# Optimization experiments

Measured on AMD Instinct MI355X. Metric: run time of the kernel, lower is better.

Reference implementation:

```python
import jax, jax.numpy as jnp
import numpy as np


def setup_inputs() -> dict:
    key = jax.random.key(0)
    kq, kk, kv, kl = jax.random.split(key, 4)
    B, Nq, Nk, D, Dv = 16, 2048, 2048, 128, 128
    queries = jax.random.normal(kq, (B, Nq, D), dtype=jnp.float32)
    keys = jax.random.normal(kk, (B, Nk, D), dtype=jnp.float32)
    values = jax.random.normal(kv, (B, Nk, Dv), dtype=jnp.float32)
    valid_lens = jax.random.randint(kl, (B,), 0, 2048, dtype=jnp.int64)
    return {"queries": queries, "keys": keys, "values": values, "valid_lens": valid_lens}


def reference(queries, keys, values, valid_lens):
    # queries: (B, Nq, d), keys: (B, Nk, d), values: (B, Nk, dv), valid_lens: (B,)
    d = queries.shape[-1]
    scores = jnp.einsum('bqd,bkd->bqk', queries, keys) / jnp.sqrt(jnp.asarray(d, queries.dtype))
    # masked_softmax: original sets masked score positions to 1e-8 (NOT -inf) before softmax
    nk = scores.shape[-1]
    mask = jnp.arange(nk)[None, :] < valid_lens[:, None]  # (B, Nk)
    scores = jnp.where(mask[:, None, :], scores, jnp.asarray(1e-8, scores.dtype))
    attn = jax.nn.softmax(scores, axis=-1)
    # dropout rate 0.0 -> identity (eval semantics)
    return jnp.einsum('bqk,bkv->bqv', attn, values)
```

## Files before the change

kernel.cpp:

```cpp
#include <hip/hip_runtime.h>
#include <stdint.h>

#define BATCH 16
#define NQ    2048
#define NK    2048
#define DD    128
#define DVV   128

typedef __bf16 bf16_t;
typedef __bf16 bf16x2 __attribute__((ext_vector_type(2)));
typedef __bf16 bf16x4 __attribute__((ext_vector_type(4)));
typedef __bf16 bf16x8 __attribute__((ext_vector_type(8)));
typedef float  f32x4  __attribute__((ext_vector_type(4)));

#define KB_OFF   ((size_t)0)
#define VT_OFF   ((size_t)8 * 1024 * 1024)
#define SUF_OFF  ((size_t)16 * 1024 * 1024)
#define SCH_OFF  (SUF_OFF + 65536)
#define WS_NEED  (SCH_OFF + 4096)

__device__ __forceinline__ int load_valid_len(const int* VL, int b) {
  bool looks64 = true;
#pragma unroll
  for (int i = 0; i < 16; ++i) {
    int hi = VL[2 * i + 1];
    unsigned lo = (unsigned)VL[2 * i];
    looks64 = looks64 && (hi == 0) && (lo <= 2048u);
  }
  int L = looks64 ? VL[2 * b] : VL[b];
  return min(max(L, 0), NK);
}

__device__ __forceinline__ void gld16(const void* g, void* l) {
  __builtin_amdgcn_global_load_lds(
      (const __attribute__((address_space(1))) unsigned int*)g,
      (__attribute__((address_space(3))) unsigned int*)l, 16, 0, 0);
}

__device__ __forceinline__ f32x4 mfma16(bf16x8 a, bf16x8 b, f32x4 c) {
  return __builtin_amdgcn_mfma_f32_16x16x32_bf16(a, b, c, 0, 0, 0);
}

__global__ void prep_kernel(const float* __restrict__ K, const float* __restrict__ V,
                            const int* __restrict__ VL,
                            bf16_t* __restrict__ Kb, bf16_t* __restrict__ Vt,
                            float* __restrict__ sufV, int* __restrict__ sched) {
  __shared__ bf16_t tile[128 * 72];
  __shared__ int bs[16];
  const int bid = blockIdx.x;
  const int t = threadIdx.x;
  if (bid < 512) {
#pragma unroll
    for (int i = 0; i < 4; ++i) {
      size_t f4 = (size_t)bid * 2048 + (size_t)i * 512 + 2 * t;
      float4 a = ((const float4*)K)[f4];
      float4 c = ((const float4*)K)[f4 + 1];
      bf16x8 o;
      o[0] = (bf16_t)a.x; o[1] = (bf16_t)a.y; o[2] = (bf16_t)a.z; o[3] = (bf16_t)a.w;
      o[4] = (bf16_t)c.x; o[5] = (bf16_t)c.y; o[6] = (bf16_t)c.z; o[7] = (bf16_t)c.w;
      ((bf16x8*)Kb)[f4 >> 1] = o;
    }
    return;
  }
  if (bid < 1024) {
    int v = bid - 512;
    int b = v & 15, kt = v >> 4;
    int L = load_valid_len(VL, b);
    int m = t & 31;
    int g = t >> 5;
    int r2 = m * 2;
    int k0g = kt * 64 + r2;
    const float* src = V + ((size_t)b * NK + k0g) * DVV;
    float sacc[4][4];
#pragma unroll
    for (int i = 0; i < 4; ++i)
#pragma unroll
      for (int j = 0; j < 4; ++j) sacc[i][j] = 0.f;
    bool a0 = (k0g >= L), a1 = (k0g + 1 >= L);
#pragma unroll
    for (int i = 0; i < 4; ++i) {
      int d4 = g * 4 + i * 32;
      float4 u0 = *(const float4*)(src + d4);
      float4 u1 = *(const float4*)(src + DVV + d4);
      *(bf16x2*)&tile[(d4 + 0) * 72 + r2] = (bf16x2){(bf16_t)u0.x, (bf16_t)u1.x};
      *(bf16x2*)&tile[(d4 + 1) * 72 + r2] = (bf16x2){(bf16_t)u0.y, (bf16_t)u1.y};
      *(bf16x2*)&tile[(d4 + 2) * 72 + r2] = (bf16x2){(bf16_t)u0.z, (bf16_t)u1.z};
      *(bf16x2*)&tile[(d4 + 3) * 72 + r2] = (bf16x2){(bf16_t)u0.w, (bf16_t)u1.w};
      if (a0) { sacc[i][0] += u0.x; sacc[i][1] += u0.y; sacc[i][2] += u0.z; sacc[i][3] += u0.w; }
      if (a1) { sacc[i][0] += u1.x; sacc[i][1] += u1.y; sacc[i][2] += u1.z; sacc[i][3] += u1.w; }
    }
    __syncthreads();
#pragma unroll
    for (int off = 1; off < 32; off <<= 1)
#pragma unroll
      for (int i = 0; i < 4; ++i)
#pragma unroll
        for (int j = 0; j < 4; ++j) sacc[i][j] += __shfl_xor(sacc[i][j], off, 64);
    if (m == 0) {
#pragma unroll
      for (int i = 0; i < 4; ++i)
#pragma unroll
        for (int j = 0; j < 4; ++j)
          atomicAdd(&sufV[b * 128 + g * 4 + i * 32 + j], sacc[i][j]);
    }
    int dv = t >> 1, half = t & 1;
    bf16_t* dst = Vt + (size_t)b * DVV * NK + (size_t)dv * NK + kt * 64 + half * 32;
    const bf16_t* srow = &tile[dv * 72 + half * 32];
#pragma unroll
    for (int j = 0; j < 4; ++j)
      *(bf16x8*)(dst + j * 8) = *(const bf16x8*)(srow + j * 8);
    return;
  }
  if (t == 0) {
    int Ls[16], idx[16];
#pragma unroll
    for (int i = 0; i < 16; ++i) { Ls[i] = load_valid_len(VL, i); idx[i] = i; }
    for (int i = 1; i < 16; ++i) {
      int lv = Ls[i], iv = idx[i], j = i - 1;
      while (j >= 0 && Ls[j] < lv) { Ls[j + 1] = Ls[j]; idx[j + 1] = idx[j]; --j; }
      Ls[j + 1] = lv; idx[j + 1] = iv;
    }
#pragma unroll
    for (int i = 0; i < 16; ++i) bs[i] = idx[i];
  }
  __syncthreads();
  for (int j = t; j < 512; j += 256) {
    int r = (j < 256) ? j : (767 - j);
    sched[j] = (bs[r >> 5] << 5) | (r & 31);
  }
}

__launch_bounds__(256, 2)
__global__ void attn_kernel(const float* __restrict__ Q, const bf16_t* __restrict__ Kb,
                            const bf16_t* __restrict__ Vt, const int* __restrict__ VL,
                            const float* __restrict__ sufV, const int* __restrict__ sched,
                            float* __restrict__ Out) {
  __shared__ __align__(16) char smem[73728];
  bf16_t* sK = (bf16_t*)smem;
  bf16_t* sV = (bf16_t*)(smem + 32768);

  const int unit = sched[blockIdx.x];
  const int b  = (unit >> 5) & 15;
  const int qt = unit & 31;
  const int L  = load_valid_len(VL, b);
  const int ktiles = (L + 63) >> 6;

  const int tid = threadIdx.x;
  const int wave = tid >> 6;
  const int lane = tid & 63;
  const int col = lane & 15;
  const int quad = lane >> 4;
  const int wr = wave >> 1;
  const int wc = wave & 1;

  bf16_t* pw = (bf16_t*)(smem + 65536 + wave * 2048);

  bf16x8 qf[2][4];
  {
    const float scq = 0.1275174307f;
#pragma unroll
    for (int m = 0; m < 2; ++m) {
      const float* qrow = Q + ((size_t)b * NQ + qt * 64 + wr * 32 + m * 16 + col) * DD + quad * 8;
#pragma unroll
      for (int ks = 0; ks < 4; ++ks) {
        float4 u0 = *(const float4*)(qrow + ks * 32);
        float4 u1 = *(const float4*)(qrow + ks * 32 + 4);
        bf16x8 f;
        f[0] = (bf16_t)(u0.x * scq); f[1] = (bf16_t)(u0.y * scq);
        f[2] = (bf16_t)(u0.z * scq); f[3] = (bf16_t)(u0.w * scq);
        f[4] = (bf16_t)(u1.x * scq); f[5] = (bf16_t)(u1.y * scq);
        f[6] = (bf16_t)(u1.z * scq); f[7] = (bf16_t)(u1.w * scq);
        qf[m][ks] = f;
      }
    }
  }

  const char* Kbyte = (const char*)Kb + (size_t)b * NK * DD * 2;
  const char* Vbyte = (const char*)Vt + (size_t)b * DVV * NK * 2;
  int koff[4], voff[4];
#pragma unroll
  for (int i = 0; i < 4; ++i) {
    int krow = wave * 16 + i * 4 + (lane >> 4);
    koff[i] = krow * 256 + (((lane & 15) ^ (krow & 15)) * 16);
    int vrow = wave * 32 + i * 8 + (lane >> 3);
    voff[i] = vrow * (NK * 2) + (((lane & 7) ^ ((lane >> 3) & 7)) * 16);
  }

  f32x4 Oacc[2][8];
#pragma unroll
  for (int m = 0; m < 2; ++m)
#pragma unroll
    for (int o = 0; o < 8; ++o) Oacc[m][o] = (f32x4){0.f, 0.f, 0.f, 0.f};
  float lsum[2][4];
#pragma unroll
  for (int m = 0; m < 2; ++m)
#pragma unroll
    for (int r = 0; r < 4; ++r) lsum[m][r] = 0.f;

  auto issueTile = [&](int kt, int bufi) {
    const char* kb = Kbyte + (size_t)kt * 16384;
    const char* vb = Vbyte + (size_t)kt * 128;
    bf16_t* kl = sK + bufi * 8192 + wave * 2048;
    bf16_t* vl = sV + bufi * 8192 + wave * 2048;
#pragma unroll
    for (int i = 0; i < 4; ++i) {
      gld16(kb + koff[i], kl + i * 512);
      gld16(vb + voff[i], vl + i * 512);
    }
  };

  if (ktiles > 0) issueTile(0, 0);
  int bufi = 0;
  for (int kt = 0; kt < ktiles; ++kt) {
    if (kt + 1 < ktiles) {
      issueTile(kt + 1, bufi ^ 1);
      asm volatile("s_waitcnt vmcnt(8)\n\ts_barrier" ::: "memory");
    } else {
      asm volatile("s_waitcnt vmcnt(0)\n\ts_barrier" ::: "memory");
    }

    const bf16_t* kb_ = sK + bufi * 8192;
    const bf16_t* vb_ = sV + bufi * 8192;

    f32x4 sc[2][2];
#pragma unroll
    for (int m = 0; m < 2; ++m)
#pragma unroll
      for (int nt = 0; nt < 2; ++nt) sc[m][nt] = (f32x4){0.f, 0.f, 0.f, 0.f};
#pragma unroll
    for (int ks = 0; ks < 4; ++ks) {
#pragma unroll
      for (int nt = 0; nt < 2; ++nt) {
        bf16x8 bb = *(const bf16x8*)&kb_[(wc * 32 + nt * 16 + col) * 128 + (((ks * 4 + quad) ^ col) * 8)];
        sc[0][nt] = mfma16(qf[0][ks], bb, sc[0][nt]);
        sc[1][nt] = mfma16(qf[1][ks], bb, sc[1][nt]);
      }
    }

    const int key0 = kt * 64 + wc * 32;
#pragma unroll
    for (int nt = 0; nt < 2; ++nt) {
      bool valid = (key0 + nt * 16 + col) < L;
#pragma unroll
      for (int m = 0; m < 2; ++m)
#pragma unroll
        for (int r = 0; r < 4; ++r) {
          float p = __builtin_amdgcn_exp2f(sc[m][nt][r]);
          p = valid ? p : 0.f;
          lsum[m][r] += p;
          int prow = quad * 4 + r;
          int cidx = m * 4 + nt * 2 + (col >> 3);
          int phys = cidx ^ (prow & 7);
          pw[prow * 64 + phys * 8 + (col & 7)] = (bf16_t)p;
        }
    }

    bf16x8 pa[2];
#pragma unroll
    for (int m = 0; m < 2; ++m)
      pa[m] = *(const bf16x8*)&pw[col * 64 + (((m * 4 + quad) ^ (col & 7)) * 8)];
#pragma unroll
    for (int o = 0; o < 8; ++o) {
      bf16x8 bb = *(const bf16x8*)&vb_[(o * 16 + col) * 64 + (((wc * 4 + quad) ^ (col & 7)) * 8)];
      Oacc[0][o] = mfma16(pa[0], bb, Oacc[0][o]);
      Oacc[1][o] = mfma16(pa[1], bb, Oacc[1][o]);
    }
    asm volatile("s_barrier" ::: "memory");
    bufi ^= 1;
  }

#pragma unroll
  for (int off = 1; off < 16; off <<= 1)
#pragma unroll
    for (int m = 0; m < 2; ++m)
#pragma unroll
      for (int r = 0; r < 4; ++r) lsum[m][r] += __shfl_xor(lsum[m][r], off, 64);

  float* scrO = (float*)(smem + wr * 18432);
  float* scrL = (float*)(smem + 65536) + wr * 32;

  if (wc == 1) {
#pragma unroll
    for (int m = 0; m < 2; ++m)
#pragma unroll
      for (int o = 0; o < 8; ++o)
        *(f32x4*)&scrO[(o * 16 + col) * 36 + m * 16 + quad * 4] = Oacc[m][o];
    if (col == 0) {
#pragma unroll
      for (int m = 0; m < 2; ++m)
#pragma unroll
        for (int r = 0; r < 4; ++r) scrL[m * 16 + quad * 4 + r] = lsum[m][r];
    }
  }
  __syncthreads();
  if (wc == 0) {
    const float wmask = (float)(NK - L);
    float invl[2][4];
#pragma unroll
    for (int m = 0; m < 2; ++m)
#pragma unroll
      for (int r = 0; r < 4; ++r)
        invl[m][r] = 1.0f / (lsum[m][r] + scrL[m * 16 + quad * 4 + r] + wmask);
    const float* sfv = sufV + b * DVV;
    float* Ob = Out + ((size_t)b * NQ + qt * 64 + wr * 32) * DVV;
#pragma unroll
    for (int m = 0; m < 2; ++m)
#pragma unroll
      for (int o = 0; o < 8; ++o) {
        f32x4 part = *(const f32x4*)&scrO[(o * 16 + col) * 36 + m * 16 + quad * 4];
        float svv = sfv[o * 16 + col];
#pragma unroll
        for (int r = 0; r < 4; ++r)
          Ob[(size_t)(m * 16 + quad * 4 + r) * DVV + o * 16 + col] =
              (Oacc[m][o][r] + part[r] + svv) * invl[m][r];
      }
  }
}

#define KSTR 152
#define VSTR 88
#define PSTR 72

__global__ void suffix_fb(const float* __restrict__ V, const int* __restrict__ VL,
                          float* __restrict__ ws) {
  int b = blockIdx.x;
  int kc = blockIdx.y;
  int L = load_valid_len(VL, b);
  int k0 = kc * 128, k1 = k0 + 128;
  int lo = max(L, k0);
  int t = threadIdx.x;
  int dv = t & 127;
  int h = t >> 7;
  float s = 0.f;
  for (int k = lo + h; k < k1; k += 2)
    s += V[((size_t)b * NK + k) * DVV + dv];
  __shared__ float part[128];
  if (h == 0) part[dv] = s;
  __syncthreads();
  if (h == 1) atomicAdd(&ws[b * DVV + dv], part[dv] + s);
}

__launch_bounds__(256, 2)
__global__ void attn_fb(const float* __restrict__ Q, const float* __restrict__ K,
                        const float* __restrict__ V, const int* __restrict__ VL,
                        const float* __restrict__ sufV, float* __restrict__ Out) {
  const int flat = blockIdx.x;
  const int b  = flat & 15;
  const int qt = flat >> 4;
  const int L  = load_valid_len(VL, b);

  __shared__ bf16_t sK2[64 * KSTR];
  __shared__ bf16_t sVT2[128 * VSTR];
  __shared__ bf16_t sP2[4 * 16 * PSTR];

  const int tid  = threadIdx.x;
  const int wave = tid >> 6;
  const int lane = tid & 63;
  const int col  = lane & 15;
  const int quad = lane >> 4;

  const float* Qb = Q + ((size_t)b * NQ + qt * 64 + wave * 16) * DD;
  const float* Kb = K + (size_t)b * NK * DD;
  const float* Vb = V + (size_t)b * NK * DVV;

  bf16x8 qf[4];
  {
    const float scq = 0.08838834764831845f;
    const float* qrow = Qb + (size_t)col * DD + quad * 8;
#pragma unroll
    for (int ks = 0; ks < 4; ++ks) {
      float4 u0 = *(const float4*)(qrow + ks * 32);
      float4 u1 = *(const float4*)(qrow + ks * 32 + 4);
      bf16x8 f;
      f[0] = (bf16_t)(u0.x * scq); f[1] = (bf16_t)(u0.y * scq);
      f[2] = (bf16_t)(u0.z * scq); f[3] = (bf16_t)(u0.w * scq);
      f[4] = (bf16_t)(u1.x * scq); f[5] = (bf16_t)(u1.y * scq);
      f[6] = (bf16_t)(u1.z * scq); f[7] = (bf16_t)(u1.w * scq);
      qf[ks] = f;
    }
  }

  f32x4 Oacc[8];
#pragma unroll
  for (int o = 0; o < 8; ++o) Oacc[o] = (f32x4){0.f, 0.f, 0.f, 0.f};
  float m_i[4], l_i[4];
#pragma unroll
  for (int r = 0; r < 4; ++r) { m_i[r] = -1e30f; l_i[r] = 0.f; }

  const int ktiles = (L + 63) >> 6;
  for (int kt = 0; kt < ktiles; ++kt) {
    {
      int r0 = tid >> 5;
      int d4 = (tid & 31) * 4;
      const float* src = Kb + ((size_t)(kt * 64) + r0) * DD + d4;
#pragma unroll
      for (int i = 0; i < 8; ++i) {
        float4 u = *(const float4*)(src + (size_t)i * 8 * DD);
        bf16x4 w4 = {(bf16_t)u.x, (bf16_t)u.y, (bf16_t)u.z, (bf16_t)u.w};
        *(bf16x4*)&sK2[(r0 + i * 8) * KSTR + d4] = w4;
      }
    }
    {
      int r2 = (tid & 31) * 2;
      int dbase = (tid >> 5) * 4;
#pragma unroll
      for (int i = 0; i < 4; ++i) {
        int d4 = dbase + i * 32;
        const float* s0 = Vb + ((size_t)(kt * 64) + r2) * DVV + d4;
        float4 u0 = *(const float4*)s0;
        float4 u1 = *(const float4*)(s0 + DVV);
        *(bf16x2*)&sVT2[(d4 + 0) * VSTR + r2] = (bf16x2){(bf16_t)u0.x, (bf16_t)u1.x};
        *(bf16x2*)&sVT2[(d4 + 1) * VSTR + r2] = (bf16x2){(bf16_t)u0.y, (bf16_t)u1.y};
        *(bf16x2*)&sVT2[(d4 + 2) * VSTR + r2] = (bf16x2){(bf16_t)u0.z, (bf16_t)u1.z};
        *(bf16x2*)&sVT2[(d4 + 3) * VSTR + r2] = (bf16x2){(bf16_t)u0.w, (bf16_t)u1.w};
      }
    }
    __syncthreads();

    f32x4 sv4[4];
#pragma unroll
    for (int nt = 0; nt < 4; ++nt) sv4[nt] = (f32x4){0.f, 0.f, 0.f, 0.f};
#pragma unroll
    for (int ks = 0; ks < 4; ++ks) {
      bf16x8 a = qf[ks];
#pragma unroll
      for (int nt = 0; nt < 4; ++nt) {
        bf16x8 bb = *(const bf16x8*)&sK2[(nt * 16 + col) * KSTR + ks * 32 + quad * 8];
        sv4[nt] = mfma16(a, bb, sv4[nt]);
      }
    }

    const int key0 = kt * 64;
    float sv[4][4];
    float mloc[4] = {-1e30f, -1e30f, -1e30f, -1e30f};
#pragma unroll
    for (int nt = 0; nt < 4; ++nt) {
      int key = key0 + nt * 16 + col;
      bool valid = key < L;
#pragma unroll
      for (int r = 0; r < 4; ++r) {
        float v = valid ? sv4[nt][r] : -1e30f;
        sv[nt][r] = v;
        mloc[r] = fmaxf(mloc[r], v);
      }
    }
#pragma unroll
    for (int off = 1; off < 16; off <<= 1)
#pragma unroll
      for (int r = 0; r < 4; ++r) mloc[r] = fmaxf(mloc[r], __shfl_xor(mloc[r], off, 64));
    float al[4];
#pragma unroll
    for (int r = 0; r < 4; ++r) {
      float mn = fmaxf(m_i[r], mloc[r]);
      al[r] = __expf(m_i[r] - mn);
      m_i[r] = mn;
    }
    float lloc[4] = {0.f, 0.f, 0.f, 0.f};
#pragma unroll
    for (int nt = 0; nt < 4; ++nt)
#pragma unroll
      for (int r = 0; r < 4; ++r) {
        float p = __expf(sv[nt][r] - m_i[r]);
        sv[nt][r] = p;
        lloc[r] += p;
      }
#pragma unroll
    for (int off = 1; off < 16; off <<= 1)
#pragma unroll
      for (int r = 0; r < 4; ++r) lloc[r] += __shfl_xor(lloc[r], off, 64);
#pragma unroll
    for (int r = 0; r < 4; ++r) l_i[r] = l_i[r] * al[r] + lloc[r];
#pragma unroll
    for (int o = 0; o < 8; ++o)
#pragma unroll
      for (int r = 0; r < 4; ++r) Oacc[o][r] *= al[r];

    bf16_t* pw = &sP2[wave * 16 * PSTR];
#pragma unroll
    for (int nt = 0; nt < 4; ++nt)
#pragma unroll
      for (int r = 0; r < 4; ++r)
        pw[(quad * 4 + r) * PSTR + nt * 16 + col] = (bf16_t)sv[nt][r];

#pragma unroll
    for (int ks2 = 0; ks2 < 2; ++ks2) {
      bf16x8 a = *(const bf16x8*)&pw[(lane & 15) * PSTR + ks2 * 32 + quad * 8];
#pragma unroll
      for (int o = 0; o < 8; ++o) {
        bf16x8 bb = *(const bf16x8*)&sVT2[(o * 16 + col) * VSTR + ks2 * 32 + quad * 8];
        Oacc[o] = mfma16(a, bb, Oacc[o]);
      }
    }
    __syncthreads();
  }

  if (L < NK) {
    const float c = 1e-8f;
    const float w = (float)(NK - L);
    float a2[4], ec[4];
#pragma unroll
    for (int r = 0; r < 4; ++r) {
      float mn = fmaxf(m_i[r], c);
      a2[r] = __expf(m_i[r] - mn);
      ec[r] = __expf(c - mn);
      l_i[r] = l_i[r] * a2[r] + w * ec[r];
    }
    const float* sfv = sufV + b * DVV;
#pragma unroll
    for (int o = 0; o < 8; ++o) {
      float svv = sfv[o * 16 + col];
#pragma unroll
      for (int r = 0; r < 4; ++r) Oacc[o][r] = Oacc[o][r] * a2[r] + ec[r] * svv;
    }
  }

  float invl[4];
#pragma unroll
  for (int r = 0; r < 4; ++r) invl[r] = 1.0f / l_i[r];

  float* Ob = Out + ((size_t)b * NQ + qt * 64 + wave * 16) * DVV;
#pragma unroll
  for (int o = 0; o < 8; ++o)
#pragma unroll
    for (int r = 0; r < 4; ++r)
      Ob[(size_t)(quad * 4 + r) * DVV + o * 16 + col] = Oacc[o][r] * invl[r];
}

extern "C" void kernel_launch(void* const* d_in, const int* in_sizes, int n_in,
                              void* d_out, int out_size, void* d_ws, size_t ws_size,
                              hipStream_t stream) {
  const float* Q  = (const float*)d_in[0];
  const float* K  = (const float*)d_in[1];
  const float* V  = (const float*)d_in[2];
  const int*   VL = (const int*)d_in[3];
  float* out = (float*)d_out;

  if (ws_size >= WS_NEED) {
    char* ws = (char*)d_ws;
    bf16_t* Kb = (bf16_t*)(ws + KB_OFF);
    bf16_t* Vt = (bf16_t*)(ws + VT_OFF);
    float* sufV = (float*)(ws + SUF_OFF);
    int* sched = (int*)(ws + SCH_OFF);

    hipMemsetAsync(sufV, 0, BATCH * DVV * sizeof(float), stream);
    prep_kernel<<<1025, 256, 0, stream>>>(K, V, VL, Kb, Vt, sufV, sched);
    attn_kernel<<<512, 256, 0, stream>>>(Q, Kb, Vt, VL, sufV, sched, out);
  } else {
    float* ws = (float*)d_ws;
    hipMemsetAsync(ws, 0, BATCH * DVV * sizeof(float), stream);
    dim3 g1(BATCH, 16);
    suffix_fb<<<g1, 256, 0, stream>>>(V, VL, ws);
    attn_fb<<<BATCH * (NQ / 64), 256, 0, stream>>>(Q, K, V, VL, ws, out);
  }
}
```

Baseline: 139.0 us.

## Widen attention blocks to 8 waves splitting 128-key tiles four ways

```diff
diff --git a/kernel.cpp b/kernel.cpp
--- a/kernel.cpp
+++ b/kernel.cpp
@@ -124,36 +124,34 @@
     for (int i = 0; i < 16; ++i) bs[i] = idx[i];
   }
   __syncthreads();
-  for (int j = t; j < 512; j += 256) {
-    int r = (j < 256) ? j : (767 - j);
-    sched[j] = (bs[r >> 5] << 5) | (r & 31);
-  }
-}
-
-__launch_bounds__(256, 2)
+  for (int j = t; j < 512; j += 256)
+    sched[j] = (bs[j >> 5] << 5) | (j & 31);
+}
+
+__launch_bounds__(512, 1)
 __global__ void attn_kernel(const float* __restrict__ Q, const bf16_t* __restrict__ Kb,
                             const bf16_t* __restrict__ Vt, const int* __restrict__ VL,
                             const float* __restrict__ sufV, const int* __restrict__ sched,
                             float* __restrict__ Out) {
-  __shared__ __align__(16) char smem[73728];
+  __shared__ __align__(16) char smem[147456];
   bf16_t* sK = (bf16_t*)smem;
-  bf16_t* sV = (bf16_t*)(smem + 32768);
+  bf16_t* sV = (bf16_t*)(smem + 65536);
 
   const int unit = sched[blockIdx.x];
   const int b  = (unit >> 5) & 15;
   const int qt = unit & 31;
   const int L  = load_valid_len(VL, b);
-  const int ktiles = (L + 63) >> 6;
+  const int ktiles = (L + 127) >> 7;
 
   const int tid = threadIdx.x;
   const int wave = tid >> 6;
   const int lane = tid & 63;
   const int col = lane & 15;
   const int quad = lane >> 4;
-  const int wr = wave >> 1;
-  const int wc = wave & 1;
-
-  bf16_t* pw = (bf16_t*)(smem + 65536 + wave * 2048);
+  const int wr = wave >> 2;
+  const int wc = wave & 3;
+
+  bf16_t* pw = (bf16_t*)(smem + 131072 + wave * 2048);
 
   bf16x8 qf[2][4];
   {
@@ -182,8 +180,8 @@
   for (int i = 0; i < 4; ++i) {
     int krow = wave * 16 + i * 4 + (lane >> 4);
     koff[i] = krow * 256 + (((lane & 15) ^ (krow & 15)) * 16);
-    int vrow = wave * 32 + i * 8 + (lane >> 3);
-    voff[i] = vrow * (NK * 2) + (((lane & 7) ^ ((lane >> 3) & 7)) * 16);
+    int vrow = wave * 16 + i * 4 + (lane >> 4);
+    voff[i] = vrow * (NK * 2) + (((lane & 15) ^ (vrow & 15)) * 16);
   }
 
   f32x4 Oacc[2][8];
@@ -198,10 +196,10 @@
     for (int r = 0; r < 4; ++r) lsum[m][r] = 0.f;
 
   auto issueTile = [&](int kt, int bufi) {
-    const char* kb = Kbyte + (size_t)kt * 16384;
-    const char* vb = Vbyte + (size_t)kt * 128;
-    bf16_t* kl = sK + bufi * 8192 + wave * 2048;
-    bf16_t* vl = sV + bufi * 8192 + wave * 2048;
+    const char* kb = Kbyte + (size_t)kt * 32768;
+    const char* vb = Vbyte + (size_t)kt * 256;
+    bf16_t* kl = sK + bufi * 16384 + wave * 2048;
+    bf16_t* vl = sV + bufi * 16384 + wave * 2048;
 #pragma unroll
     for (int i = 0; i < 4; ++i) {
       gld16(kb + koff[i], kl + i * 512);
@@ -219,8 +217,8 @@
       asm volatile("s_waitcnt vmcnt(0)\n\ts_barrier" ::: "memory");
     }
 
-    const bf16_t* kb_ = sK + bufi * 8192;
-    const bf16_t* vb_ = sV + bufi * 8192;
+    const bf16_t* kb_ = sK + bufi * 16384;
+    const bf16_t* vb_ = sV + bufi * 16384;
 
     f32x4 sc[2][2];
 #pragma unroll
@@ -237,7 +235,7 @@
       }
     }
 
-    const int key0 = kt * 64 + wc * 32;
+    const int key0 = kt * 128 + wc * 32;
 #pragma unroll
     for (int nt = 0; nt < 2; ++nt) {
       bool valid = (key0 + nt * 16 + col) < L;
@@ -261,7 +259,7 @@
       pa[m] = *(const bf16x8*)&pw[col * 64 + (((m * 4 + quad) ^ (col & 7)) * 8)];
 #pragma unroll
     for (int o = 0; o < 8; ++o) {
-      bf16x8 bb = *(const bf16x8*)&vb_[(o * 16 + col) * 64 + (((wc * 4 + quad) ^ (col & 7)) * 8)];
+      bf16x8 bb = *(const bf16x8*)&vb_[(o * 16 + col) * 128 + (((wc * 4 + quad) ^ col) * 8)];
       Oacc[0][o] = mfma16(pa[0], bb, Oacc[0][o]);
       Oacc[1][o] = mfma16(pa[1], bb, Oacc[1][o]);
     }
@@ -276,10 +274,9 @@
 #pragma unroll
       for (int r = 0; r < 4; ++r) lsum[m][r] += __shfl_xor(lsum[m][r], off, 64);
 
-  float* scrO = (float*)(smem + wr * 18432);
-  float* scrL = (float*)(smem + 65536) + wr * 32;
-
-  if (wc == 1) {
+  if (wc) {
+    float* scrO = (float*)smem + (size_t)(wr * 3 + (wc - 1)) * 4608;
+    float* scrL = (float*)(smem + 131072) + (wr * 3 + (wc - 1)) * 32;
 #pragma unroll
     for (int m = 0; m < 2; ++m)
 #pragma unroll
@@ -299,20 +296,29 @@
 #pragma unroll
     for (int m = 0; m < 2; ++m)
 #pragma unroll
-      for (int r = 0; r < 4; ++r)
-        invl[m][r] = 1.0f / (lsum[m][r] + scrL[m * 16 + quad * 4 + r] + wmask);
+      for (int r = 0; r < 4; ++r) {
+        float lt = lsum[m][r] + wmask;
+#pragma unroll
+        for (int s = 0; s < 3; ++s)
+          lt += ((float*)(smem + 131072))[(wr * 3 + s) * 32 + m * 16 + quad * 4 + r];
+        invl[m][r] = 1.0f / lt;
+      }
     const float* sfv = sufV + b * DVV;
     float* Ob = Out + ((size_t)b * NQ + qt * 64 + wr * 32) * DVV;
 #pragma unroll
     for (int m = 0; m < 2; ++m)
 #pragma unroll
       for (int o = 0; o < 8; ++o) {
-        f32x4 part = *(const f32x4*)&scrO[(o * 16 + col) * 36 + m * 16 + quad * 4];
+        f32x4 acc = Oacc[m][o];
+#pragma unroll
+        for (int s = 0; s < 3; ++s)
+          acc += *(const f32x4*)&((float*)smem)[(size_t)(wr * 3 + s) * 4608 +
+                                               (o * 16 + col) * 36 + m * 16 + quad * 4];
         float svv = sfv[o * 16 + col];
 #pragma unroll
         for (int r = 0; r < 4; ++r)
           Ob[(size_t)(m * 16 + quad * 4 + r) * DVV + o * 16 + col] =
-              (Oacc[m][o][r] + part[r] + svv) * invl[m][r];
+              (acc[r] + svv) * invl[m][r];
       }
   }
 }
@@ -544,7 +550,7 @@
 
     hipMemsetAsync(sufV, 0, BATCH * DVV * sizeof(float), stream);
     prep_kernel<<<1025, 256, 0, stream>>>(K, V, VL, Kb, Vt, sufV, sched);
-    attn_kernel<<<512, 256, 0, stream>>>(Q, Kb, Vt, VL, sufV, sched, out);
+    attn_kernel<<<512, 512, 0, stream>>>(Q, Kb, Vt, VL, sufV, sched, out);
   } else {
     float* ws = (float*)d_ws;
     hipMemsetAsync(ws, 0, BATCH * DVV * sizeof(float), stream);
```

Measured after the change: 146.4 us. +5.3%, slower.

## Use 8 waves per block with 16-row query groups and MFMA priority hints

Applied to the files above, without the earlier changes.

```diff
diff --git a/kernel.cpp b/kernel.cpp
--- a/kernel.cpp
+++ b/kernel.cpp
@@ -124,18 +124,16 @@
     for (int i = 0; i < 16; ++i) bs[i] = idx[i];
   }
   __syncthreads();
-  for (int j = t; j < 512; j += 256) {
-    int r = (j < 256) ? j : (767 - j);
-    sched[j] = (bs[r >> 5] << 5) | (r & 31);
-  }
-}
-
-__launch_bounds__(256, 2)
+  for (int j = t; j < 512; j += 256)
+    sched[j] = (bs[j >> 5] << 5) | (j & 31);
+}
+
+__launch_bounds__(512, 4)
 __global__ void attn_kernel(const float* __restrict__ Q, const bf16_t* __restrict__ Kb,
                             const bf16_t* __restrict__ Vt, const int* __restrict__ VL,
                             const float* __restrict__ sufV, const int* __restrict__ sched,
                             float* __restrict__ Out) {
-  __shared__ __align__(16) char smem[73728];
+  __shared__ __align__(16) char smem[81920];
   bf16_t* sK = (bf16_t*)smem;
   bf16_t* sV = (bf16_t*)(smem + 32768);
 
@@ -150,60 +148,51 @@
   const int lane = tid & 63;
   const int col = lane & 15;
   const int quad = lane >> 4;
-  const int wr = wave >> 1;
-  const int wc = wave & 1;
+  const int qg = wave >> 1;
+  const int kg = wave & 1;
 
   bf16_t* pw = (bf16_t*)(smem + 65536 + wave * 2048);
 
-  bf16x8 qf[2][4];
+  bf16x8 qf[4];
   {
     const float scq = 0.1275174307f;
-#pragma unroll
-    for (int m = 0; m < 2; ++m) {
-      const float* qrow = Q + ((size_t)b * NQ + qt * 64 + wr * 32 + m * 16 + col) * DD + quad * 8;
-#pragma unroll
-      for (int ks = 0; ks < 4; ++ks) {
-        float4 u0 = *(const float4*)(qrow + ks * 32);
-        float4 u1 = *(const float4*)(qrow + ks * 32 + 4);
-        bf16x8 f;
-        f[0] = (bf16_t)(u0.x * scq); f[1] = (bf16_t)(u0.y * scq);
-        f[2] = (bf16_t)(u0.z * scq); f[3] = (bf16_t)(u0.w * scq);
-        f[4] = (bf16_t)(u1.x * scq); f[5] = (bf16_t)(u1.y * scq);
-        f[6] = (bf16_t)(u1.z * scq); f[7] = (bf16_t)(u1.w * scq);
-        qf[m][ks] = f;
-      }
+    const float* qrow = Q + ((size_t)b * NQ + qt * 64 + qg * 16 + col) * DD + quad * 8;
+#pragma unroll
+    for (int ks = 0; ks < 4; ++ks) {
+      float4 u0 = *(const float4*)(qrow + ks * 32);
+      float4 u1 = *(const float4*)(qrow + ks * 32 + 4);
+      bf16x8 f;
+      f[0] = (bf16_t)(u0.x * scq); f[1] = (bf16_t)(u0.y * scq);
+      f[2] = (bf16_t)(u0.z * scq); f[3] = (bf16_t)(u0.w * scq);
+      f[4] = (bf16_t)(u1.x * scq); f[5] = (bf16_t)(u1.y * scq);
+      f[6] = (bf16_t)(u1.z * scq); f[7] = (bf16_t)(u1.w * scq);
+      qf[ks] = f;
     }
   }
 
   const char* Kbyte = (const char*)Kb + (size_t)b * NK * DD * 2;
   const char* Vbyte = (const char*)Vt + (size_t)b * DVV * NK * 2;
-  int koff[4], voff[4];
-#pragma unroll
-  for (int i = 0; i < 4; ++i) {
-    int krow = wave * 16 + i * 4 + (lane >> 4);
+  int koff[2], voff[2];
+#pragma unroll
+  for (int i = 0; i < 2; ++i) {
+    int krow = wave * 8 + i * 4 + quad;
     koff[i] = krow * 256 + (((lane & 15) ^ (krow & 15)) * 16);
-    int vrow = wave * 32 + i * 8 + (lane >> 3);
-    voff[i] = vrow * (NK * 2) + (((lane & 7) ^ ((lane >> 3) & 7)) * 16);
-  }
-
-  f32x4 Oacc[2][8];
-#pragma unroll
-  for (int m = 0; m < 2; ++m)
-#pragma unroll
-    for (int o = 0; o < 8; ++o) Oacc[m][o] = (f32x4){0.f, 0.f, 0.f, 0.f};
-  float lsum[2][4];
-#pragma unroll
-  for (int m = 0; m < 2; ++m)
-#pragma unroll
-    for (int r = 0; r < 4; ++r) lsum[m][r] = 0.f;
+    int vrow = wave * 16 + i * 8 + (lane >> 3);
+    voff[i] = vrow * (NK * 2) + (((lane & 7) ^ (vrow & 7)) * 16);
+  }
+
+  f32x4 Oacc[8];
+#pragma unroll
+  for (int o = 0; o < 8; ++o) Oacc[o] = (f32x4){0.f, 0.f, 0.f, 0.f};
+  float lsum[4] = {0.f, 0.f, 0.f, 0.f};
 
   auto issueTile = [&](int kt, int bufi) {
     const char* kb = Kbyte + (size_t)kt * 16384;
     const char* vb = Vbyte + (size_t)kt * 128;
-    bf16_t* kl = sK + bufi * 8192 + wave * 2048;
-    bf16_t* vl = sV + bufi * 8192 + wave * 2048;
-#pragma unroll
-    for (int i = 0; i < 4; ++i) {
+    bf16_t* kl = sK + bufi * 8192 + wave * 1024;
+    bf16_t* vl = sV + bufi * 8192 + wave * 1024;
+#pragma unroll
+    for (int i = 0; i < 2; ++i) {
       gld16(kb + koff[i], kl + i * 512);
       gld16(vb + voff[i], vl + i * 512);
     }
@@ -214,7 +203,7 @@
   for (int kt = 0; kt < ktiles; ++kt) {
     if (kt + 1 < ktiles) {
       issueTile(kt + 1, bufi ^ 1);
-      asm volatile("s_waitcnt vmcnt(8)\n\ts_barrier" ::: "memory");
+      asm volatile("s_waitcnt vmcnt(4)\n\ts_barrier" ::: "memory");
     } else {
       asm volatile("s_waitcnt vmcnt(0)\n\ts_barrier" ::: "memory");
     }
@@ -222,49 +211,44 @@
     const bf16_t* kb_ = sK + bufi * 8192;
     const bf16_t* vb_ = sV + bufi * 8192;
 
-    f32x4 sc[2][2];
-#pragma unroll
-    for (int m = 0; m < 2; ++m)
-#pragma unroll
-      for (int nt = 0; nt < 2; ++nt) sc[m][nt] = (f32x4){0.f, 0.f, 0.f, 0.f};
+    f32x4 sc[2];
+#pragma unroll
+    for (int nt = 0; nt < 2; ++nt) sc[nt] = (f32x4){0.f, 0.f, 0.f, 0.f};
+    __builtin_amdgcn_s_setprio(1);
 #pragma unroll
     for (int ks = 0; ks < 4; ++ks) {
 #pragma unroll
       for (int nt = 0; nt < 2; ++nt) {
-        bf16x8 bb = *(const bf16x8*)&kb_[(wc * 32 + nt * 16 + col) * 128 + (((ks * 4 + quad) ^ col) * 8)];
-        sc[0][nt] = mfma16(qf[0][ks], bb, sc[0][nt]);
-        sc[1][nt] = mfma16(qf[1][ks], bb, sc[1][nt]);
-      }
-    }
-
-    const int key0 = kt * 64 + wc * 32;
+        bf16x8 bb = *(const bf16x8*)&kb_[(kg * 32 + nt * 16 + col) * 128 + (((ks * 4 + quad) ^ col) * 8)];
+        sc[nt] = mfma16(qf[ks], bb, sc[nt]);
+      }
+    }
+    __builtin_amdgcn_s_setprio(0);
+
+    const int key0 = kt * 64 + kg * 32;
 #pragma unroll
     for (int nt = 0; nt < 2; ++nt) {
       bool valid = (key0 + nt * 16 + col) < L;
 #pragma unroll
-      for (int m = 0; m < 2; ++m)
-#pragma unroll
-        for (int r = 0; r < 4; ++r) {
-          float p = __builtin_amdgcn_exp2f(sc[m][nt][r]);
-          p = valid ? p : 0.f;
-          lsum[m][r] += p;
-          int prow = quad * 4 + r;
-          int cidx = m * 4 + nt * 2 + (col >> 3);
-          int phys = cidx ^ (prow & 7);
-          pw[prow * 64 + phys * 8 + (col & 7)] = (bf16_t)p;
-        }
-    }
-
-    bf16x8 pa[2];
-#pragma unroll
-    for (int m = 0; m < 2; ++m)
-      pa[m] = *(const bf16x8*)&pw[col * 64 + (((m * 4 + quad) ^ (col & 7)) * 8)];
+      for (int r = 0; r < 4; ++r) {
+        float p = __builtin_amdgcn_exp2f(sc[nt][r]);
+        p = valid ? p : 0.f;
+        lsum[r] += p;
+        int prow = quad * 4 + r;
+        int cidx = nt * 2 + (col >> 3);
+        int phys = cidx ^ (prow & 7);
+        pw[prow * 64 + phys * 8 + (col & 7)] = (bf16_t)p;
+      }
+    }
+
+    bf16x8 pa = *(const bf16x8*)&pw[col * 64 + ((quad ^ (col & 7)) * 8)];
+    __builtin_amdgcn_s_setprio(1);
 #pragma unroll
     for (int o = 0; o < 8; ++o) {
-      bf16x8 bb = *(const bf16x8*)&vb_[(o * 16 + col) * 64 + (((wc * 4 + quad) ^ (col & 7)) * 8)];
-      Oacc[0][o] = mfma16(pa[0], bb, Oacc[0][o]);
-      Oacc[1][o] = mfma16(pa[1], bb, Oacc[1][o]);
-    }
+      bf16x8 bb = *(const bf16x8*)&vb_[(o * 16 + col) * 64 + (((kg * 4 + quad) ^ (col & 7)) * 8)];
+      Oacc[o] = mfma16(pa, bb, Oacc[o]);
+    }
+    __builtin_amdgcn_s_setprio(0);
     asm volatile("s_barrier" ::: "memory");
     bufi ^= 1;
   }
@@ -272,48 +256,38 @@
 #pragma unroll
   for (int off = 1; off < 16; off <<= 1)
 #pragma unroll
-    for (int m = 0; m < 2; ++m)
-#pragma unroll
-      for (int r = 0; r < 4; ++r) lsum[m][r] += __shfl_xor(lsum[m][r], off, 64);
-
-  float* scrO = (float*)(smem + wr * 18432);
-  float* scrL = (float*)(smem + 65536) + wr * 32;
-
-  if (wc == 1) {
-#pragma unroll
-    for (int m = 0; m < 2; ++m)
-#pragma unroll
-      for (int o = 0; o < 8; ++o)
-        *(f32x4*)&scrO[(o * 16 + col) * 36 + m * 16 + quad * 4] = Oacc[m][o];
+    for (int r = 0; r < 4; ++r) lsum[r] += __shfl_xor(lsum[r], off, 64);
+
+  float* scrO = (float*)smem + qg * 2560;
+  float* scrL = (float*)(smem + 65536) + qg * 16;
+
+  if (kg) {
+#pragma unroll
+    for (int o = 0; o < 8; ++o)
+      *(f32x4*)&scrO[(o * 16 + col) * 20 + quad * 4] = Oacc[o];
     if (col == 0) {
 #pragma unroll
-      for (int m = 0; m < 2; ++m)
-#pragma unroll
-        for (int r = 0; r < 4; ++r) scrL[m * 16 + quad * 4 + r] = lsum[m][r];
+      for (int r = 0; r < 4; ++r) scrL[quad * 4 + r] = lsum[r];
     }
   }
   __syncthreads();
-  if (wc == 0) {
+  if (!kg) {
     const float wmask = (float)(NK - L);
-    float invl[2][4];
-#pragma unroll
-    for (int m = 0; m < 2; ++m)
+    float invl[4];
+#pragma unroll
+    for (int r = 0; r < 4; ++r)
+      invl[r] = 1.0f / (lsum[r] + scrL[quad * 4 + r] + wmask);
+    const float* sfv = sufV + b * DVV;
+    float* Ob = Out + ((size_t)b * NQ + qt * 64 + qg * 16) * DVV;
+#pragma unroll
+    for (int o = 0; o < 8; ++o) {
+      f32x4 part = *(const f32x4*)&scrO[(o * 16 + col) * 20 + quad * 4];
+      float svv = sfv[o * 16 + col];
 #pragma unroll
       for (int r = 0; r < 4; ++r)
-        invl[m][r] = 1.0f / (lsum[m][r] + scrL[m * 16 + quad * 4 + r] + wmask);
-    const float* sfv = sufV + b * DVV;
-    float* Ob = Out + ((size_t)b * NQ + qt * 64 + wr * 32) * DVV;
-#pragma unroll
-    for (int m = 0; m < 2; ++m)
-#pragma unroll
-      for (int o = 0; o < 8; ++o) {
-        f32x4 part = *(const f32x4*)&scrO[(o * 16 + col) * 36 + m * 16 + quad * 4];
-        float svv = sfv[o * 16 + col];
-#pragma unroll
-        for (int r = 0; r < 4; ++r)
-          Ob[(size_t)(m * 16 + quad * 4 + r) * DVV + o * 16 + col] =
-              (Oacc[m][o][r] + part[r] + svv) * invl[m][r];
-      }
+        Ob[(size_t)(quad * 4 + r) * DVV + o * 16 + col] =
+            (Oacc[o][r] + part[r] + svv) * invl[r];
+    }
   }
 }
 
@@ -544,7 +518,7 @@
 
     hipMemsetAsync(sufV, 0, BATCH * DVV * sizeof(float), stream);
     prep_kernel<<<1025, 256, 0, stream>>>(K, V, VL, Kb, Vt, sufV, sched);
-    attn_kernel<<<512, 256, 0, stream>>>(Q, Kb, Vt, VL, sufV, sched, out);
+    attn_kernel<<<512, 512, 0, stream>>>(Q, Kb, Vt, VL, sufV, sched, out);
   } else {
     float* ws = (float*)d_ws;
     hipMemsetAsync(ws, 0, BATCH * DVV * sizeof(float), stream);
```

Result: no change. 140.3 us (+0.9%).
